# Kernel tuning notes

Measured on AMD Instinct MI355X. Metric: run time of the kernel, lower is better.

The kernel has to match this reference:

```python
import jax, jax.numpy as jnp
import numpy as np

B, L, N = 32, 4096, 256
FFT_K = 5
MAX_FREQ_LEVELS = 4
LAGS = [1, 3, 6, 12, 24]


def setup_inputs() -> dict:
    key = jax.random.key(0)
    k0, k1, k2, k3, k4 = jax.random.split(key, 5)
    x = jax.random.normal(k0, (B, L, N), dtype=jnp.float32)
    # depth_gate: Linear(2->8), GELU, Linear(8->1)  (stored as x @ W + b)
    dg_w1 = jax.random.normal(k1, (2, 8), dtype=jnp.float32) * 0.5
    dg_b1 = jax.random.normal(k2, (8,), dtype=jnp.float32) * 0.1
    dg_w2 = jax.random.normal(k3, (8, 1), dtype=jnp.float32) * 0.3
    dg_b2 = jax.random.normal(k4, (1,), dtype=jnp.float32) * 0.1
    return {"x": x, "dg_w1": dg_w1, "dg_b1": dg_b1, "dg_w2": dg_w2, "dg_b2": dg_b2}


def reference(x, dg_w1, dg_b1, dg_w2, dg_b2):
    eps = 1e-8
    # ---- moment statistics (over time dim=1), torch.std is unbiased (ddof=1) ----
    mean = x.mean(axis=1, keepdims=True)                     # (B,1,N)
    std = jnp.std(x, axis=1, ddof=1, keepdims=True)          # (B,1,N)
    std_e = std + eps
    diff = x - mean
    skew = (diff ** 3).mean(axis=1, keepdims=True) / (std_e ** 3 + eps)
    kurt = (diff ** 4).mean(axis=1, keepdims=True) / (std_e ** 4 + eps) - 3.0

    # ---- FFT features with iterative multi-level top-k extraction ----
    amp = jnp.abs(jnp.fft.rfft(x, axis=1))                   # (B,F,N)
    F_bins = amp.shape[1]
    freqs = jnp.arange(F_bins, dtype=jnp.float32) / L        # (F,)
    amp_T = jnp.transpose(amp, (0, 2, 1))                    # (B,N,F)

    residual = amp_T
    aggregated = jnp.zeros_like(amp_T)
    total_energy = amp_T.mean(axis=-1, keepdims=True) + eps
    running = jnp.ones((B, N, 1), dtype=x.dtype)
    bidx = jnp.arange(B)[:, None, None]
    nidx = jnp.arange(N)[None, :, None]
    for level in range(MAX_FREQ_LEVELS):
        k_level = min(max(1, int(round(FFT_K / 2 ** level))), F_bins)
        level_amp, level_idx = jax.lax.top_k(residual, k_level)
        level_map = jnp.zeros_like(residual).at[bidx, nidx, level_idx].set(level_amp)
        residual_ratio = residual.mean(axis=-1, keepdims=True) / total_energy
        level_ratio = jnp.full_like(residual_ratio, float(level + 1) / MAX_FREQ_LEVELS)
        gate_in = jnp.concatenate([residual_ratio, level_ratio], axis=-1)    # (B,N,2)
        h = jax.nn.gelu(gate_in @ dg_w1 + dg_b1, approximate=False)
        need_deeper = jax.nn.sigmoid(h @ dg_w2 + dg_b2)                      # (B,N,1)
        aggregated = aggregated + running * level_map
        residual = residual - level_map
        running = running * need_deeper

    # hard top-k decode
    top_amp, top_idx = jax.lax.top_k(aggregated, FFT_K)      # (B,N,k)
    top_freqs = freqs[top_idx]                               # (B,N,k)
    max_amp = amp_T.max(axis=-1, keepdims=True) + eps
    top_amp_norm = top_amp / (max_amp + eps)
    fft_feat = jnp.concatenate([top_freqs, top_amp_norm], axis=-1)   # (B,N,2k)
    fft_feat = jnp.transpose(fft_feat, (0, 2, 1))                    # (B,2k,N)

    # ---- autocorrelation at fixed lags ----
    x_norm = diff / std_e
    ac = jnp.stack(
        [(x_norm[:, :-lag, :] * x_norm[:, lag:, :]).mean(axis=1) for lag in LAGS],
        axis=1,
    )  # (B, n_lags, N)

    feats = jnp.concatenate([mean, std, skew, kurt, fft_feat, ac], axis=1)  # (B,19,N)
    return jnp.transpose(feats, (0, 2, 1))  # (B,N,19)
```

## Files before the change

kernel.cpp:

```cpp
#include <hip/hip_runtime.h>
#include <math.h>

#define B_    32
#define L_    4096
#define N_    256
#define NC    2048
#define NSEG  16
#define SEGLEN (L_ / NSEG)
#define CHUNK 32
#define NQ    9

__global__ __launch_bounds__(256) void k_transpose(const float* __restrict__ x,
                                                   float* __restrict__ xt) {
  __shared__ float tile[32][33];
  const int b  = blockIdx.z;
  const int l0 = blockIdx.x * 32;
  const int n0 = blockIdx.y * 32;
  const int tx = threadIdx.x;
  const int ty = threadIdx.y;
#pragma unroll
  for (int k = 0; k < 4; ++k) {
    const int l = l0 + ty + 8 * k;
    tile[ty + 8 * k][tx] = x[((size_t)b * L_ + l) * N_ + (n0 + tx)];
  }
  __syncthreads();
#pragma unroll
  for (int k = 0; k < 4; ++k) {
    const int n = n0 + ty + 8 * k;
    xt[((size_t)b * N_ + n) * L_ + (l0 + tx)] = tile[tx][ty + 8 * k];
  }
}

__global__ __launch_bounds__(256) void k_stats_partial(const float* __restrict__ x,
                                                       float* __restrict__ P) {
  const int s = blockIdx.x;
  const int b = blockIdx.y;
  const int n = threadIdx.x;
  const int l0 = s * SEGLEN;
  const float* xp = x + (size_t)b * L_ * N_ + n;

  float prev[CHUNK];
#pragma unroll
  for (int j = 0; j < CHUNK; ++j) {
    const int l = l0 - CHUNK + j;
    prev[j] = (l >= 0) ? xp[(size_t)l * N_] : 0.0f;
  }
  float s1 = 0.f, s2 = 0.f, s3 = 0.f, s4 = 0.f;
  float c1 = 0.f, c3 = 0.f, c6 = 0.f, c12 = 0.f, c24 = 0.f;
  for (int c = 0; c < SEGLEN / CHUNK; ++c) {
    float cur[CHUNK];
    const int lb = l0 + c * CHUNK;
#pragma unroll
    for (int j = 0; j < CHUNK; ++j) cur[j] = xp[(size_t)(lb + j) * N_];
#pragma unroll
    for (int j = 0; j < CHUNK; ++j) {
      const float v = cur[j], v2 = v * v;
      s1 += v; s2 += v2; s3 += v2 * v; s4 += v2 * v2;
    }
#pragma unroll
    for (int j = 0; j < CHUNK; ++j) {
      const float v = cur[j];
      c1  += v * ((j >= 1)  ? cur[j - 1]  : prev[CHUNK + j - 1]);
      c3  += v * ((j >= 3)  ? cur[j - 3]  : prev[CHUNK + j - 3]);
      c6  += v * ((j >= 6)  ? cur[j - 6]  : prev[CHUNK + j - 6]);
      c12 += v * ((j >= 12) ? cur[j - 12] : prev[CHUNK + j - 12]);
      c24 += v * ((j >= 24) ? cur[j - 24] : prev[CHUNK + j - 24]);
    }
#pragma unroll
    for (int j = 0; j < CHUNK; ++j) prev[j] = cur[j];
  }
  float* Pp = P + (size_t)(s * B_ + b) * NQ * N_ + n;
  Pp[0 * N_] = s1; Pp[1 * N_] = s2; Pp[2 * N_] = s3; Pp[3 * N_] = s4;
  Pp[4 * N_] = c1; Pp[5 * N_] = c3; Pp[6 * N_] = c6; Pp[7 * N_] = c12; Pp[8 * N_] = c24;
}

__global__ __launch_bounds__(256) void k_stats_final(const float* __restrict__ x,
                                                     const float* __restrict__ P,
                                                     float* __restrict__ out) {
  const int b = blockIdx.x;
  const int n = threadIdx.x;
  float S[NQ];
#pragma unroll
  for (int q = 0; q < NQ; ++q) S[q] = 0.0f;
  for (int s = 0; s < NSEG; ++s) {
    const float* Pp = P + (size_t)(s * B_ + b) * NQ * N_ + n;
#pragma unroll
    for (int q = 0; q < NQ; ++q) S[q] += Pp[q * N_];
  }
  const float Lf = (float)L_;
  const float mu = S[0] / Lf;
  float ssd = S[1] - Lf * mu * mu;
  ssd = fmaxf(ssd, 0.0f);
  const float stdv = sqrtf(ssd / (Lf - 1.0f));
  const float se  = stdv + 1e-8f;
  const float m3 = (S[2] - 3.0f * mu * S[1] + 2.0f * Lf * mu * mu * mu) / Lf;
  const float m4 = (S[3] - 4.0f * mu * S[2] + 6.0f * mu * mu * S[1]
                    - 3.0f * Lf * mu * mu * mu * mu) / Lf;
  const float se2 = se * se;
  const float skew = m3 / (se2 * se + 1e-8f);
  const float kurt = m4 / (se2 * se2 + 1e-8f) - 3.0f;

  const float* xp = x + (size_t)b * L_ * N_ + n;
  float hl[5], tl[5];
  {
    float hs = 0.0f, ts = 0.0f;
#pragma unroll
    for (int t = 0; t < 24; ++t) {
      hs += xp[(size_t)t * N_];
      ts += xp[(size_t)(L_ - 1 - t) * N_];
      if (t == 0)  { hl[0] = hs; tl[0] = ts; }
      if (t == 2)  { hl[1] = hs; tl[1] = ts; }
      if (t == 5)  { hl[2] = hs; tl[2] = ts; }
      if (t == 11) { hl[3] = hs; tl[3] = ts; }
      if (t == 23) { hl[4] = hs; tl[4] = ts; }
    }
  }
  float* op = out + ((size_t)b * N_ + n) * 19;
  op[0] = mu; op[1] = stdv; op[2] = skew; op[3] = kurt;
  const int lags[5] = {1, 3, 6, 12, 24};
  const float inv_se2 = 1.0f / se2;
#pragma unroll
  for (int i = 0; i < 5; ++i) {
    const float cnt = (float)(L_ - lags[i]);
    const float SA = S[0] - tl[i];
    const float SB = S[0] - hl[i];
    const float num = S[4 + i] - mu * (SA + SB) + cnt * mu * mu;
    op[14 + i] = num * inv_se2 / cnt;
  }
}

__global__ __launch_bounds__(256) void k_fft_top(const float* __restrict__ base, int stride,
                                                 float* __restrict__ out) {
  __shared__ float A[2 * NC];
  __shared__ float Bb[2 * NC];
  __shared__ float TW[NC];
  const int tid = threadIdx.x;
  const int bn  = blockIdx.x;
  const float* src = (stride == 1)
      ? base + (size_t)bn * L_
      : base + (size_t)(bn >> 8) * ((size_t)L_ * N_) + (bn & (N_ - 1));

  float* twr = TW;
  float* twi = TW + NC / 2;
  for (int t = tid; t < NC / 2; t += 256) {
    float sv, cv;
    sincosf(-6.283185307179586f * (float)t / (float)NC, &sv, &cv);
    twr[t] = cv; twi[t] = sv;
  }
  if (stride == 1) {
    const float2* s2 = (const float2*)src;
    for (int i = tid; i < NC; i += 256) {
      const float2 v = s2[i];
      A[i] = v.x; A[NC + i] = v.y;
    }
  } else {
    for (int i = tid; i < NC; i += 256) {
      A[i]      = src[(size_t)(2 * i)     * N_];
      A[NC + i] = src[(size_t)(2 * i + 1) * N_];
    }
  }
  __syncthreads();

  float* xr = A;  float* xi = A + NC;
  float* yr = Bb; float* yi = Bb + NC;
  for (int s = 1; s < NC; s <<= 1) {
    for (int i = tid; i < NC / 2; i += 256) {
      const int tb = i & ~(s - 1);
      const float ar = xr[i],          ai = xi[i];
      const float br = xr[i + NC / 2], bi = xi[i + NC / 2];
      const float wr = twr[tb], wi = twi[tb];
      const float dr = ar - br, di = ai - bi;
      yr[i + tb]     = ar + br;
      yi[i + tb]     = ai + bi;
      yr[i + tb + s] = dr * wr - di * wi;
      yi[i + tb + s] = dr * wi + di * wr;
    }
    __syncthreads();
    float* t;
    t = xr; xr = yr; yr = t;
    t = xi; xi = yi; yi = t;
  }
  float* amp = yr;

  for (int k = tid; k <= NC; k += 256) {
    const int ki = k & (NC - 1);
    const int kr = (NC - k) & (NC - 1);
    const float zar = xr[ki], zai = xi[ki];
    const float zbr = xr[kr], zbi = -xi[kr];
    const float Er = 0.5f * (zar + zbr);
    const float Ei = 0.5f * (zai + zbi);
    const float dr = zar - zbr, di = zai - zbi;
    const float Or = 0.5f * di;
    const float Oi = -0.5f * dr;
    float sv, cv;
    sincosf(-6.283185307179586f * (float)k / (float)L_, &sv, &cv);
    const float Xr = Er + cv * Or - sv * Oi;
    const float Xi = Ei + cv * Oi + sv * Or;
    amp[k] = sqrtf(Xr * Xr + Xi * Xi);
  }
  __syncthreads();

  float* redv = TW;
  int*   redi = (int*)(TW + NC / 2);
  float* topv = TW + 256;
  int*   topi = (int*)(TW + NC / 2 + 256);
  for (int r = 0; r < 5; ++r) {
    float bv = -1.0f; int bi = 1 << 30;
    for (int k = tid; k <= NC; k += 256) {
      const float v = amp[k];
      if (v > bv) { bv = v; bi = k; }
    }
    redv[tid] = bv; redi[tid] = bi;
    __syncthreads();
    for (int off = 128; off > 0; off >>= 1) {
      if (tid < off) {
        const float v2 = redv[tid + off];
        const int   i2 = redi[tid + off];
        if (v2 > redv[tid] || (v2 == redv[tid] && i2 < redi[tid])) {
          redv[tid] = v2; redi[tid] = i2;
        }
      }
      __syncthreads();
    }
    if (tid == 0) {
      topv[r] = redv[0];
      topi[r] = redi[0];
      amp[redi[0]] = -1.0f;
    }
    __syncthreads();
  }
  if (tid == 0) {
    float* op = out + (size_t)bn * 19;
    const float den = topv[0] + 2e-8f;
#pragma unroll
    for (int r = 0; r < 5; ++r) {
      op[4 + r] = (float)topi[r] * (1.0f / (float)L_);
      op[9 + r] = topv[r] / den;
    }
  }
}

extern "C" void kernel_launch(void* const* d_in, const int* in_sizes, int n_in,
                              void* d_out, int out_size, void* d_ws, size_t ws_size,
                              hipStream_t stream) {
  const float* x = (const float*)d_in[0];
  float* out = (float*)d_out;
  float* ws  = (float*)d_ws;

  const size_t xt_elems   = (size_t)B_ * N_ * L_;
  const size_t part_elems = (size_t)NSEG * B_ * NQ * N_;
  const bool use_xt = ws_size >= (xt_elems + part_elems) * sizeof(float);
  float* xt = ws;
  float* P  = use_xt ? (ws + xt_elems) : ws;

  if (use_xt) {
    k_transpose<<<dim3(L_ / 32, N_ / 32, B_), dim3(32, 8), 0, stream>>>(x, xt);
  }
  k_stats_partial<<<dim3(NSEG, B_), 256, 0, stream>>>(x, P);
  k_stats_final<<<B_, 256, 0, stream>>>(x, P, out);
  if (use_xt) {
    k_fft_top<<<B_ * N_, 256, 0, stream>>>(xt, 1, out);
  } else {
    k_fft_top<<<B_ * N_, 256, 0, stream>>>(x, N_, out);
  }
}
```

Before: 394.2 us.

## Fuse transpose into stats pass and replace radix-2 FFT with register radix-8 FFT

The standalone transpose kernel is removed and its work folded into the stats kernel, which now writes the time-major copy from a shared tile, with the segment count doubled. The radix-2 shared-memory FFT with eleven synchronized stages becomes a register-resident radix-8/8/8/4 FFT with padded shared indexing and fewer barriers. Top-k selection now uses wavefront shuffles, takes 8 candidates, and recomputes exact double-precision DFT bins when near-ties are detected. The refinement path adds costly double-precision work for blocks that hit ties, and the higher register pressure under the new occupancy hint may limit the gain.

Result: faster. 353.4 us (-10.4%).

```diff
diff --git a/kernel.cpp b/kernel.cpp
--- a/kernel.cpp
+++ b/kernel.cpp
@@ -5,39 +5,26 @@
 #define L_    4096
 #define N_    256
 #define NC    2048
-#define NSEG  16
+#define NSEG  32
 #define SEGLEN (L_ / NSEG)
 #define CHUNK 32
+#define NCH   (SEGLEN / CHUNK)
 #define NQ    9
-
-__global__ __launch_bounds__(256) void k_transpose(const float* __restrict__ x,
-                                                   float* __restrict__ xt) {
-  __shared__ float tile[32][33];
-  const int b  = blockIdx.z;
-  const int l0 = blockIdx.x * 32;
-  const int n0 = blockIdx.y * 32;
-  const int tx = threadIdx.x;
-  const int ty = threadIdx.y;
-#pragma unroll
-  for (int k = 0; k < 4; ++k) {
-    const int l = l0 + ty + 8 * k;
-    tile[ty + 8 * k][tx] = x[((size_t)b * L_ + l) * N_ + (n0 + tx)];
-  }
-  __syncthreads();
-#pragma unroll
-  for (int k = 0; k < 4; ++k) {
-    const int n = n0 + ty + 8 * k;
-    xt[((size_t)b * N_ + n) * L_ + (l0 + tx)] = tile[tx][ty + 8 * k];
-  }
-}
-
-__global__ __launch_bounds__(256) void k_stats_partial(const float* __restrict__ x,
-                                                       float* __restrict__ P) {
+#define NCAND 8
+
+__device__ __forceinline__ int PD(int i) { return i + (i >> 3); }
+
+__global__ __launch_bounds__(256, 4) void k_stats_trans(const float* __restrict__ x,
+                                                        float* __restrict__ P,
+                                                        float* __restrict__ xt,
+                                                        int do_t) {
+  __shared__ float tile[CHUNK][N_ + 1];
   const int s = blockIdx.x;
   const int b = blockIdx.y;
   const int n = threadIdx.x;
   const int l0 = s * SEGLEN;
   const float* xp = x + (size_t)b * L_ * N_ + n;
+  float* xtb = xt + (size_t)b * N_ * L_;
 
   float prev[CHUNK];
 #pragma unroll
@@ -47,9 +34,9 @@
   }
   float s1 = 0.f, s2 = 0.f, s3 = 0.f, s4 = 0.f;
   float c1 = 0.f, c3 = 0.f, c6 = 0.f, c12 = 0.f, c24 = 0.f;
-  for (int c = 0; c < SEGLEN / CHUNK; ++c) {
+  for (int c = 0; c < NCH; ++c) {
+    const int lb = l0 + c * CHUNK;
     float cur[CHUNK];
-    const int lb = l0 + c * CHUNK;
 #pragma unroll
     for (int j = 0; j < CHUNK; ++j) cur[j] = xp[(size_t)(lb + j) * N_];
 #pragma unroll
@@ -65,6 +52,24 @@
       c6  += v * ((j >= 6)  ? cur[j - 6]  : prev[CHUNK + j - 6]);
       c12 += v * ((j >= 12) ? cur[j - 12] : prev[CHUNK + j - 12]);
       c24 += v * ((j >= 24) ? cur[j - 24] : prev[CHUNK + j - 24]);
+    }
+    if (do_t) {
+#pragma unroll
+      for (int j = 0; j < CHUNK; ++j) tile[j][n] = cur[j];
+      __syncthreads();
+#pragma unroll
+      for (int it = 0; it < 8; ++it) {
+        const int g  = n + 256 * it;
+        const int np = g >> 3;
+        const int j4 = g & 7;
+        float4 w;
+        w.x = tile[4 * j4 + 0][np];
+        w.y = tile[4 * j4 + 1][np];
+        w.z = tile[4 * j4 + 2][np];
+        w.w = tile[4 * j4 + 3][np];
+        *(float4*)(xtb + (size_t)np * L_ + lb + 4 * j4) = w;
+      }
+      __syncthreads();
     }
 #pragma unroll
     for (int j = 0; j < CHUNK; ++j) prev[j] = cur[j];
@@ -129,113 +134,286 @@
   }
 }
 
-__global__ __launch_bounds__(256) void k_fft_top(const float* __restrict__ base, int stride,
-                                                 float* __restrict__ out) {
-  __shared__ float A[2 * NC];
-  __shared__ float Bb[2 * NC];
-  __shared__ float TW[NC];
+__device__ __forceinline__ void dft8(float (&vr)[8], float (&vi)[8]) {
+  const float C7 = 0.70710678118654752f;
+  float t0r = vr[0] + vr[4], t0i = vi[0] + vi[4];
+  float t1r = vr[0] - vr[4], t1i = vi[0] - vi[4];
+  float t2r = vr[2] + vr[6], t2i = vi[2] + vi[6];
+  float t3r = vr[2] - vr[6], t3i = vi[2] - vi[6];
+  float E0r = t0r + t2r, E0i = t0i + t2i;
+  float E2r = t0r - t2r, E2i = t0i - t2i;
+  float E1r = t1r + t3i, E1i = t1i - t3r;
+  float E3r = t1r - t3i, E3i = t1i + t3r;
+  float u0r = vr[1] + vr[5], u0i = vi[1] + vi[5];
+  float u1r = vr[1] - vr[5], u1i = vi[1] - vi[5];
+  float u2r = vr[3] + vr[7], u2i = vi[3] + vi[7];
+  float u3r = vr[3] - vr[7], u3i = vi[3] - vi[7];
+  float O0r = u0r + u2r, O0i = u0i + u2i;
+  float O2r = u0r - u2r, O2i = u0i - u2i;
+  float O1r = u1r + u3i, O1i = u1i - u3r;
+  float O3r = u1r - u3i, O3i = u1i + u3r;
+  vr[0] = E0r + O0r; vi[0] = E0i + O0i;
+  vr[4] = E0r - O0r; vi[4] = E0i - O0i;
+  float a1r = C7 * (O1r + O1i), a1i = C7 * (O1i - O1r);
+  vr[1] = E1r + a1r; vi[1] = E1i + a1i;
+  vr[5] = E1r - a1r; vi[5] = E1i - a1i;
+  vr[2] = E2r + O2i; vi[2] = E2i - O2r;
+  vr[6] = E2r - O2i; vi[6] = E2i + O2r;
+  float a3r = C7 * (O3i - O3r), a3i = -C7 * (O3r + O3i);
+  vr[3] = E3r + a3r; vi[3] = E3i + a3i;
+  vr[7] = E3r - a3r; vi[7] = E3i - a3i;
+}
+
+__device__ __forceinline__ void twid8(float (&vr)[8], float (&vi)[8], float w1r, float w1i) {
+  float w2r = w1r * w1r - w1i * w1i, w2i = 2.f * w1r * w1i;
+  float w3r = w2r * w1r - w2i * w1i, w3i = w2r * w1i + w2i * w1r;
+  float w4r = w2r * w2r - w2i * w2i, w4i = 2.f * w2r * w2i;
+  float w5r = w3r * w2r - w3i * w2i, w5i = w3r * w2i + w3i * w2r;
+  float w6r = w3r * w3r - w3i * w3i, w6i = 2.f * w3r * w3i;
+  float w7r = w4r * w3r - w4i * w3i, w7i = w4r * w3i + w4i * w3r;
+  float t;
+  t = vr[1] * w1r - vi[1] * w1i; vi[1] = vr[1] * w1i + vi[1] * w1r; vr[1] = t;
+  t = vr[2] * w2r - vi[2] * w2i; vi[2] = vr[2] * w2i + vi[2] * w2r; vr[2] = t;
+  t = vr[3] * w3r - vi[3] * w3i; vi[3] = vr[3] * w3i + vi[3] * w3r; vr[3] = t;
+  t = vr[4] * w4r - vi[4] * w4i; vi[4] = vr[4] * w4i + vi[4] * w4r; vr[4] = t;
+  t = vr[5] * w5r - vi[5] * w5i; vi[5] = vr[5] * w5i + vi[5] * w5r; vr[5] = t;
+  t = vr[6] * w6r - vi[6] * w6i; vi[6] = vr[6] * w6i + vi[6] * w6r; vr[6] = t;
+  t = vr[7] * w7r - vi[7] * w7i; vi[7] = vr[7] * w7i + vi[7] * w7r; vr[7] = t;
+}
+
+__global__ __launch_bounds__(256, 4) void k_fft_top(const float* __restrict__ base, int stride,
+                                                    float* __restrict__ out) {
+  __shared__ float XR[2304];
+  __shared__ float XI[2304];
+  __shared__ float TWR[256];
+  __shared__ float TWI[256];
+  __shared__ float RV[4];
+  __shared__ int   RI[4];
+  __shared__ float TOPV[NCAND];
+  __shared__ int   TOPI[NCAND];
+  __shared__ double DA[NCAND];
+  __shared__ int REFINE;
   const int tid = threadIdx.x;
   const int bn  = blockIdx.x;
-  const float* src = (stride == 1)
-      ? base + (size_t)bn * L_
-      : base + (size_t)(bn >> 8) * ((size_t)L_ * N_) + (bn & (N_ - 1));
-
-  float* twr = TW;
-  float* twi = TW + NC / 2;
-  for (int t = tid; t < NC / 2; t += 256) {
-    float sv, cv;
-    sincosf(-6.283185307179586f * (float)t / (float)NC, &sv, &cv);
-    twr[t] = cv; twi[t] = sv;
-  }
+
+  float sn, cn;
+  sincosf(-6.283185307179586f * (float)tid / 2048.0f, &sn, &cn);
+  TWR[tid] = cn; TWI[tid] = sn;
+  float tb4r, tb4i;
+  {
+    float s4, c4;
+    sincosf(-6.283185307179586f * (float)tid / 4096.0f, &s4, &c4);
+    tb4r = c4; tb4i = s4;
+  }
+
+  float vr[8], vi[8];
   if (stride == 1) {
-    const float2* s2 = (const float2*)src;
-    for (int i = tid; i < NC; i += 256) {
-      const float2 v = s2[i];
-      A[i] = v.x; A[NC + i] = v.y;
+    const float2* src2 = (const float2*)(base + (size_t)bn * L_);
+#pragma unroll
+    for (int r = 0; r < 8; ++r) {
+      const float2 v = src2[tid + 256 * r];
+      vr[r] = v.x; vi[r] = v.y;
     }
   } else {
-    for (int i = tid; i < NC; i += 256) {
-      A[i]      = src[(size_t)(2 * i)     * N_];
-      A[NC + i] = src[(size_t)(2 * i + 1) * N_];
-    }
+    const float* src = base + (size_t)(bn >> 8) * ((size_t)L_ * N_) + (bn & (N_ - 1));
+#pragma unroll
+    for (int r = 0; r < 8; ++r) {
+      vr[r] = src[(size_t)(2 * (tid + 256 * r)) * N_];
+      vi[r] = src[(size_t)(2 * (tid + 256 * r) + 1) * N_];
+    }
+  }
+
+  dft8(vr, vi);
+  twid8(vr, vi, cn, sn);
+#pragma unroll
+  for (int m = 0; m < 8; ++m) {
+    XR[PD(8 * tid + m)] = vr[m];
+    XI[PD(8 * tid + m)] = vi[m];
   }
   __syncthreads();
 
-  float* xr = A;  float* xi = A + NC;
-  float* yr = Bb; float* yi = Bb + NC;
-  for (int s = 1; s < NC; s <<= 1) {
-    for (int i = tid; i < NC / 2; i += 256) {
-      const int tb = i & ~(s - 1);
-      const float ar = xr[i],          ai = xi[i];
-      const float br = xr[i + NC / 2], bi = xi[i + NC / 2];
-      const float wr = twr[tb], wi = twi[tb];
-      const float dr = ar - br, di = ai - bi;
-      yr[i + tb]     = ar + br;
-      yi[i + tb]     = ai + bi;
-      yr[i + tb + s] = dr * wr - di * wi;
-      yi[i + tb + s] = dr * wi + di * wr;
-    }
-    __syncthreads();
-    float* t;
-    t = xr; xr = yr; yr = t;
-    t = xi; xi = yi; yi = t;
-  }
-  float* amp = yr;
-
-  for (int k = tid; k <= NC; k += 256) {
-    const int ki = k & (NC - 1);
-    const int kr = (NC - k) & (NC - 1);
-    const float zar = xr[ki], zai = xi[ki];
-    const float zbr = xr[kr], zbi = -xi[kr];
-    const float Er = 0.5f * (zar + zbr);
-    const float Ei = 0.5f * (zai + zbi);
-    const float dr = zar - zbr, di = zai - zbi;
-    const float Or = 0.5f * di;
-    const float Oi = -0.5f * dr;
-    float sv, cv;
-    sincosf(-6.283185307179586f * (float)k / (float)L_, &sv, &cv);
+#pragma unroll
+  for (int st = 0; st < 2; ++st) {
+    const int s = (st == 0) ? 8 : 64;
+#pragma unroll
+    for (int r = 0; r < 8; ++r) {
+      vr[r] = XR[PD(tid + 256 * r)];
+      vi[r] = XI[PD(tid + 256 * r)];
+    }
+    __syncthreads();
+    const int tb = tid & ~(s - 1);
+    dft8(vr, vi);
+    twid8(vr, vi, TWR[tb], TWI[tb]);
+    const int wb = tid + 7 * tb;
+#pragma unroll
+    for (int m = 0; m < 8; ++m) {
+      XR[PD(wb + m * s)] = vr[m];
+      XI[PD(wb + m * s)] = vi[m];
+    }
+    __syncthreads();
+  }
+
+  {
+    float ar[8], ai[8];
+#pragma unroll
+    for (int h = 0; h < 2; ++h) {
+      const int i = tid + 256 * h;
+#pragma unroll
+      for (int r = 0; r < 4; ++r) {
+        ar[4 * h + r] = XR[PD(i + 512 * r)];
+        ai[4 * h + r] = XI[PD(i + 512 * r)];
+      }
+    }
+    __syncthreads();
+#pragma unroll
+    for (int h = 0; h < 2; ++h) {
+      const int i = tid + 256 * h;
+      const float x0r = ar[4*h+0], x0i = ai[4*h+0], x1r = ar[4*h+1], x1i = ai[4*h+1];
+      const float x2r = ar[4*h+2], x2i = ai[4*h+2], x3r = ar[4*h+3], x3i = ai[4*h+3];
+      const float t0r = x0r + x2r, t0i = x0i + x2i;
+      const float t1r = x0r - x2r, t1i = x0i - x2i;
+      const float t2r = x1r + x3r, t2i = x1i + x3i;
+      const float t3r = x1r - x3r, t3i = x1i - x3i;
+      XR[PD(i)]        = t0r + t2r;  XI[PD(i)]        = t0i + t2i;
+      XR[PD(i + 512)]  = t1r + t3i;  XI[PD(i + 512)]  = t1i - t3r;
+      XR[PD(i + 1024)] = t0r - t2r;  XI[PD(i + 1024)] = t0i - t2i;
+      XR[PD(i + 1536)] = t1r - t3i;  XI[PD(i + 1536)] = t1i + t3r;
+    }
+    __syncthreads();
+  }
+
+  const float WAC[9] = {1.f, 0.92387953f, 0.70710678f, 0.38268343f, 0.f,
+                        -0.38268343f, -0.70710678f, -0.92387953f, -1.f};
+  const float WAS[9] = {0.f, 0.38268343f, 0.70710678f, 0.92387953f, 1.f,
+                        0.92387953f, 0.70710678f, 0.38268343f, 0.f};
+  float av[8];
+#pragma unroll
+  for (int j = 0; j < 8; ++j) {
+    const int k  = tid + 256 * j;
+    const int kr = (2048 - k) & 2047;
+    const float zar = XR[PD(k)],  zai = XI[PD(k)];
+    const float zbr = XR[PD(kr)], zbi = -XI[PD(kr)];
+    const float Er = 0.5f * (zar + zbr), Ei = 0.5f * (zai + zbi);
+    const float Or = 0.5f * (zai - zbi), Oi = -0.5f * (zar - zbr);
+    const float cv = WAC[j] * tb4r + WAS[j] * tb4i;
+    const float sv = WAC[j] * tb4i - WAS[j] * tb4r;
     const float Xr = Er + cv * Or - sv * Oi;
     const float Xi = Ei + cv * Oi + sv * Or;
-    amp[k] = sqrtf(Xr * Xr + Xi * Xi);
-  }
+    av[j] = sqrtf(Xr * Xr + Xi * Xi);
+  }
+  float a2048 = 0.f;
+  if (tid == 0) a2048 = fabsf(XR[0] - XI[0]);
   __syncthreads();
-
-  float* redv = TW;
-  int*   redi = (int*)(TW + NC / 2);
-  float* topv = TW + 256;
-  int*   topi = (int*)(TW + NC / 2 + 256);
-  for (int r = 0; r < 5; ++r) {
-    float bv = -1.0f; int bi = 1 << 30;
-    for (int k = tid; k <= NC; k += 256) {
+  float* amp = XR;
+#pragma unroll
+  for (int j = 0; j < 8; ++j) amp[tid + 256 * j] = av[j];
+  if (tid == 0) amp[2048] = a2048;
+  __syncthreads();
+
+  const int lane = tid & 63, wid = tid >> 6;
+  for (int rr = 0; rr < NCAND; ++rr) {
+    float bv = -1.f; int bi = 1 << 30;
+#pragma unroll
+    for (int j = 0; j < 8; ++j) {
+      const int k = tid + 256 * j;
       const float v = amp[k];
       if (v > bv) { bv = v; bi = k; }
     }
-    redv[tid] = bv; redi[tid] = bi;
-    __syncthreads();
-    for (int off = 128; off > 0; off >>= 1) {
-      if (tid < off) {
-        const float v2 = redv[tid + off];
-        const int   i2 = redi[tid + off];
-        if (v2 > redv[tid] || (v2 == redv[tid] && i2 < redi[tid])) {
-          redv[tid] = v2; redi[tid] = i2;
+    if (tid == 0) {
+      const float v = amp[2048];
+      if (v > bv) { bv = v; bi = 2048; }
+    }
+#pragma unroll
+    for (int off = 32; off > 0; off >>= 1) {
+      const float v2 = __shfl_down(bv, off);
+      const int   i2 = __shfl_down(bi, off);
+      if (v2 > bv || (v2 == bv && i2 < bi)) { bv = v2; bi = i2; }
+    }
+    if (lane == 0) { RV[wid] = bv; RI[wid] = bi; }
+    __syncthreads();
+    if (tid == 0) {
+      float mv = RV[0]; int mi = RI[0];
+#pragma unroll
+      for (int w = 1; w < 4; ++w) {
+        if (RV[w] > mv || (RV[w] == mv && RI[w] < mi)) { mv = RV[w]; mi = RI[w]; }
+      }
+      TOPV[rr] = mv; TOPI[rr] = mi;
+      amp[mi] = -1.f;
+    }
+    __syncthreads();
+  }
+
+  if (tid == 0) {
+    int need = 0;
+    const float thr = 1e-3f * TOPV[0];
+#pragma unroll
+    for (int r = 0; r < 5; ++r) {
+      if (TOPV[r] - TOPV[r + 1] < thr) need = 1;
+    }
+    REFINE = need;
+  }
+  __syncthreads();
+
+  if (REFINE) {
+    const int g = tid >> 5;
+    const int j = tid & 31;
+    const int k = TOPI[g];
+    const int t0 = 128 * j;
+    const int e0 = (int)(((long long)k * (long long)t0) & 4095LL);
+    double sp, cp;  sincos(-2.0 * 3.14159265358979323846 * (double)e0 / 4096.0, &sp, &cp);
+    double sw, cw;  sincos(-2.0 * 3.14159265358979323846 * (double)k  / 4096.0, &sw, &cw);
+    double ar = 0.0, ai = 0.0;
+    if (stride == 1) {
+      const float* xr_ = base + (size_t)bn * L_ + t0;
+      for (int t = 0; t < 128; ++t) {
+        const double xv = (double)xr_[t];
+        ar += xv * cp; ai += xv * sp;
+        const double ncp = cp * cw - sp * sw;
+        sp = cp * sw + sp * cw; cp = ncp;
+      }
+    } else {
+      const float* xr_ = base + (size_t)(bn >> 8) * ((size_t)L_ * N_) + (bn & (N_ - 1));
+      for (int t = 0; t < 128; ++t) {
+        const double xv = (double)xr_[(size_t)(t0 + t) * N_];
+        ar += xv * cp; ai += xv * sp;
+        const double ncp = cp * cw - sp * sw;
+        sp = cp * sw + sp * cw; cp = ncp;
+      }
+    }
+#pragma unroll
+    for (int off = 16; off > 0; off >>= 1) {
+      ar += __shfl_down(ar, off, 32);
+      ai += __shfl_down(ai, off, 32);
+    }
+    if (j == 0) DA[g] = sqrt(ar * ar + ai * ai);
+    __syncthreads();
+    if (tid == 0) {
+      double da[NCAND]; int di[NCAND];
+#pragma unroll
+      for (int r = 0; r < NCAND; ++r) { da[r] = DA[r]; di[r] = TOPI[r]; }
+      for (int i2 = 1; i2 < NCAND; ++i2) {
+        const double v = da[i2]; const int ii = di[i2];
+        int p = i2 - 1;
+        while (p >= 0 && (da[p] < v || (da[p] == v && di[p] > ii))) {
+          da[p + 1] = da[p]; di[p + 1] = di[p]; --p;
         }
-      }
-      __syncthreads();
-    }
-    if (tid == 0) {
-      topv[r] = redv[0];
-      topi[r] = redi[0];
-      amp[redi[0]] = -1.0f;
-    }
-    __syncthreads();
-  }
-  if (tid == 0) {
+        da[p + 1] = v; di[p + 1] = ii;
+      }
+      float* op = out + (size_t)bn * 19;
+      const double den = da[0] + 2e-8;
+#pragma unroll
+      for (int r = 0; r < 5; ++r) {
+        op[4 + r] = (float)di[r] * (1.0f / (float)L_);
+        op[9 + r] = (float)(da[r] / den);
+      }
+    }
+  } else if (tid == 0) {
     float* op = out + (size_t)bn * 19;
-    const float den = topv[0] + 2e-8f;
+    const float den = TOPV[0] + 2e-8f;
 #pragma unroll
     for (int r = 0; r < 5; ++r) {
-      op[4 + r] = (float)topi[r] * (1.0f / (float)L_);
-      op[9 + r] = topv[r] / den;
+      op[4 + r] = (float)TOPI[r] * (1.0f / (float)L_);
+      op[9 + r] = TOPV[r] / den;
     }
   }
 }
@@ -253,10 +431,8 @@
   float* xt = ws;
   float* P  = use_xt ? (ws + xt_elems) : ws;
 
-  if (use_xt) {
-    k_transpose<<<dim3(L_ / 32, N_ / 32, B_), dim3(32, 8), 0, stream>>>(x, xt);
-  }
-  k_stats_partial<<<dim3(NSEG, B_), 256, 0, stream>>>(x, P);
+  k_stats_trans<<<dim3(NSEG, B_), 256, 0, stream>>>(x, P, use_xt ? xt : nullptr,
+                                                    use_xt ? 1 : 0);
   k_stats_final<<<B_, 256, 0, stream>>>(x, P, out);
   if (use_xt) {
     k_fft_top<<<B_ * N_, 256, 0, stream>>>(xt, 1, out);
```
